# Kernel optimization log

Measured on AMD Instinct MI355X. Metric: run time of the kernel, lower is better.

## Reference

```python
import jax, jax.numpy as jnp
import numpy as np

EPS = 1e-8

@jax.custom_vjp
def spike(x):
    # Heaviside forward, SuperSpike surrogate gradient in backward
    return (x > 0.0).astype(x.dtype)

def _spike_fwd(x):
    return spike(x), x

def _spike_bwd(x, g):
    return (g / (1.0 + 10.0 * jnp.abs(x)) ** 2,)

spike.defvjp(_spike_fwd, _spike_bwd)


def setup_inputs() -> dict:
    key = jax.random.key(0)
    k1, k2, k3, k4 = jax.random.split(key, 4)
    B, T, I, O = 128, 128, 1024, 1024
    x = jax.random.normal(k1, (B, T, I), dtype=jnp.float32)
    # w ~ N(0, 1/sqrt(I)) per reset_parameters
    w = jax.random.normal(k2, (I, O), dtype=jnp.float32) * np.float32(1.0 / np.sqrt(I))
    # beta ~ N(0.7, 0.01), clamped to [0,1]
    beta = jnp.clip(0.7 + 0.01 * jax.random.normal(k3, (1,), dtype=jnp.float32), 0.0, 1.0)
    # b ~ N(1.0, 0.01), clamped to >= 0
    b = jnp.clip(1.0 + 0.01 * jax.random.normal(k4, (1024,), dtype=jnp.float32), 0.0, None)
    return {"x": x, "w": w, "beta": beta, "b": b}


def reference(x, w, beta, b):
    # x: [B, T, I]; w: [I, O]; beta: [1]; b: [O]
    h = jnp.einsum('btc,cd->btd', x, w)                 # [B, T, O]
    d = jnp.einsum('ab,ac->bc', w, w)                    # lateral reset matrix [O, O]
    norm = (w ** 2).sum(0)                               # [O]
    inv_norm = 1.0 / (norm + EPS)
    B, O = x.shape[0], w.shape[1]

    def step(carry, h_t):
        mem, spk = carry
        rst = spk @ d                                    # [B, O]
        mem = (mem - rst) * beta + h_t * (1.0 - beta)
        mthr = mem * inv_norm - b
        spk = spike(mthr)
        return (mem, spk), spk

    init = (jnp.zeros((B, O), x.dtype), jnp.zeros((B, O), x.dtype))
    _, spk_rec = jax.lax.scan(step, init, jnp.swapaxes(h, 0, 1))  # [T, B, O]
    spk_rec = jnp.swapaxes(spk_rec, 0, 1)                # [B, T, O]
    loss = 0.5 * (spk_rec ** 2).mean()
    return spk_rec, loss
```

## Files before the change

kernel.cpp:

```cpp
#include <hip/hip_runtime.h>
#include <hip/hip_fp16.h>

#define B_ 128
#define T_ 128
#define I_ 1024
#define O_ 1024
#define M_ (B_*T_)
#define NOUT (M_*O_)

typedef __attribute__((ext_vector_type(8))) _Float16 half8;
typedef __attribute__((ext_vector_type(4))) float floatx4;

__device__ __forceinline__ void gld_lds16(const void* g, void* l) {
    __builtin_amdgcn_global_load_lds((const __attribute__((address_space(1))) void*)g,
                                     (__attribute__((address_space(3))) void*)l,
                                     16, 0, 0);
}

__device__ __forceinline__ void barrier_lds_only() {
    asm volatile("" ::: "memory");
    __builtin_amdgcn_s_waitcnt(0xC07F);
    __builtin_amdgcn_s_barrier();
    asm volatile("" ::: "memory");
}

__device__ __forceinline__ void split3h(float x, unsigned short& h,
                                        unsigned short& m, unsigned short& l) {
    __half f0 = __float2half(x);
    float r1 = x - __half2float(f0);
    __half f1 = __float2half(r1);
    float r2 = r1 - __half2float(f1);
    __half f2 = __float2half(r2);
    h = __half_as_ushort(f0);
    m = __half_as_ushort(f1);
    l = __half_as_ushort(f2);
}

__global__ __launch_bounds__(256) void split_x(const float* __restrict__ X,
                                               unsigned short* __restrict__ Xh,
                                               unsigned short* __restrict__ Xm,
                                               unsigned short* __restrict__ Xl) {
    size_t base = ((size_t)blockIdx.x * 256 + threadIdx.x) * 4;
    float4 v = *(const float4*)(X + base);
    ushort4 hh, mm, ll;
    split3h(v.x, hh.x, mm.x, ll.x);
    split3h(v.y, hh.y, mm.y, ll.y);
    split3h(v.z, hh.z, mm.z, ll.z);
    split3h(v.w, hh.w, mm.w, ll.w);
    *(ushort4*)(Xh + base) = hh;
    *(ushort4*)(Xm + base) = mm;
    *(ushort4*)(Xl + base) = ll;
}

__global__ __launch_bounds__(256) void split_wt(const float* __restrict__ W,
                                                unsigned short* __restrict__ WTh,
                                                unsigned short* __restrict__ WTm,
                                                unsigned short* __restrict__ WTl) {
    __shared__ float t[64][65];
    const int tid = threadIdx.x;
    const int tx = tid & 63, ty4 = tid >> 6;
    const int r0 = blockIdx.x * 64, c0 = blockIdx.y * 64;
#pragma unroll
    for (int j = 0; j < 16; ++j) {
        int row = j * 4 + ty4;
        t[row][tx] = W[(size_t)(r0 + row) * O_ + c0 + tx];
    }
    __syncthreads();
#pragma unroll
    for (int j = 0; j < 16; ++j) {
        int i = j * 4 + ty4;
        float v = t[tx][i];
        unsigned short h, m, l;
        split3h(v, h, m, l);
        size_t off = (size_t)(c0 + i) * I_ + r0 + tx;
        WTh[off] = h; WTm[off] = m; WTl[off] = l;
    }
}

__global__ __launch_bounds__(512, 2) void gemm_h_mfma(
        const unsigned short* __restrict__ Xh, const unsigned short* __restrict__ Xm,
        const unsigned short* __restrict__ Xl, const unsigned short* __restrict__ WTh,
        const unsigned short* __restrict__ WTm, const unsigned short* __restrict__ WTl,
        float* __restrict__ H) {
    const int K = I_, N = O_;
    __shared__ unsigned short P[2][36864];

    const int tid = threadIdx.x;
    const int lane = tid & 63;
    const int wid = tid >> 6;
    const int wrow = wid >> 2;
    const int wcol = wid & 3;
    const int l15 = lane & 15, quad = lane >> 4;
    const int bm = blockIdx.x * 128, bn = blockIdx.y * 256;

    const int srow = tid >> 2, sch = tid & 3;
    const int schg = sch ^ ((srow >> 1) & 3);
    const unsigned short* gsrcA[3];
    const unsigned short* gsrcB[3];
    gsrcA[0] = Xh  + (size_t)(bm + srow) * K + schg * 8;
    gsrcA[1] = Xm  + (size_t)(bm + srow) * K + schg * 8;
    gsrcA[2] = Xl  + (size_t)(bm + srow) * K + schg * 8;
    gsrcB[0] = WTh + (size_t)(bn + srow) * K + schg * 8;
    gsrcB[1] = WTm + (size_t)(bn + srow) * K + schg * 8;
    gsrcB[2] = WTl + (size_t)(bn + srow) * K + schg * 8;

    auto stage = [&](int kt) {
        unsigned short* wb = &P[0][0] + (size_t)(kt & 1) * 36864;
        const size_t k0 = (size_t)kt * 32;
#pragma unroll
        for (int p = 0; p < 3; ++p)
            gld_lds16(gsrcA[p] + k0, wb + p * 4096 + tid * 8);
#pragma unroll
        for (int p = 0; p < 3; ++p) {
            unsigned short* bb = wb + 12288 + p * 8192 + tid * 8;
            gld_lds16(gsrcB[p] + k0, bb);
            gld_lds16(gsrcB[p] + (size_t)128 * K + k0, bb + 4096);
        }
    };

    floatx4 acc[4][4];
#pragma unroll
    for (int mt = 0; mt < 4; ++mt)
#pragma unroll
        for (int nt = 0; nt < 4; ++nt) acc[mt][nt] = (floatx4)(0.f);

    stage(0);

    for (int kt = 0; kt < 32; ++kt) {
        const unsigned short* rb = &P[0][0] + (size_t)(kt & 1) * 36864;

        asm volatile("" ::: "memory");
        __builtin_amdgcn_s_waitcnt(0x1F70);
        __builtin_amdgcn_s_barrier();
        asm volatile("" ::: "memory");

        half8 Af[3][4];
#pragma unroll
        for (int pa = 0; pa < 3; ++pa)
#pragma unroll
            for (int mt = 0; mt < 4; ++mt) {
                const int row = wrow * 64 + mt * 16 + l15;
                const int chk = quad ^ ((row >> 1) & 3);
                Af[pa][mt] = *(const half8*)(rb + pa * 4096 + row * 32 + chk * 8);
            }

        if (kt < 31) stage(kt + 1);

#pragma unroll
        for (int pb = 0; pb < 3; ++pb) {
            half8 Bf[4];
#pragma unroll
            for (int nt = 0; nt < 4; ++nt) {
                const int col = wcol * 64 + nt * 16 + l15;
                const int chk = quad ^ ((col >> 1) & 3);
                Bf[nt] = *(const half8*)(rb + 12288 + pb * 8192 + col * 32 + chk * 8);
            }
#pragma unroll
            for (int nt = 0; nt < 4; ++nt)
#pragma unroll
                for (int mt = 0; mt < 4; ++mt) {
                    acc[mt][nt] = __builtin_amdgcn_mfma_f32_16x16x32_f16(Af[0][mt], Bf[nt], acc[mt][nt], 0, 0, 0);
                    if (pb < 2)
                        acc[mt][nt] = __builtin_amdgcn_mfma_f32_16x16x32_f16(Af[1][mt], Bf[nt], acc[mt][nt], 0, 0, 0);
                    if (pb == 0)
                        acc[mt][nt] = __builtin_amdgcn_mfma_f32_16x16x32_f16(Af[2][mt], Bf[nt], acc[mt][nt], 0, 0, 0);
                }
        }
    }

#pragma unroll
    for (int mt = 0; mt < 4; ++mt)
#pragma unroll
        for (int nt = 0; nt < 4; ++nt) {
            int grow = bm + wrow * 64 + mt * 16 + quad * 4;
            int gcol = bn + wcol * 64 + nt * 16 + l15;
            float* hp = H + (size_t)grow * N + gcol;
#pragma unroll
            for (int r = 0; r < 4; ++r) hp[(size_t)r * N] = acc[mt][nt][r];
        }
}

__global__ __launch_bounds__(256) void gemm_wtw(const float* __restrict__ W,
                                                float* __restrict__ D) {
    const int K = I_, N = O_;
    __shared__ float As[32][68];
    __shared__ float Bs[32][68];
    const int tid = threadIdx.x;
    const int tx = tid & 15, ty = tid >> 4;
    const int bj = blockIdx.x * 64, bo = blockIdx.y * 64;
    const int lr = tid >> 4;
    const int lc = (tid & 15) << 2;

    float acc[4][4];
#pragma unroll
    for (int m = 0; m < 4; m++)
#pragma unroll
        for (int n = 0; n < 4; n++) acc[m][n] = 0.f;

    for (int k0 = 0; k0 < K; k0 += 32) {
        float4 a0 = *(const float4*)(W + (size_t)(k0 + lr) * N + bj + lc);
        float4 a1 = *(const float4*)(W + (size_t)(k0 + lr + 16) * N + bj + lc);
        float4 b0 = *(const float4*)(W + (size_t)(k0 + lr) * N + bo + lc);
        float4 b1 = *(const float4*)(W + (size_t)(k0 + lr + 16) * N + bo + lc);
        __syncthreads();
        *(float4*)&As[lr][lc] = a0; *(float4*)&As[lr + 16][lc] = a1;
        *(float4*)&Bs[lr][lc] = b0; *(float4*)&Bs[lr + 16][lc] = b1;
        __syncthreads();
#pragma unroll
        for (int k = 0; k < 32; ++k) {
            float4 av = *(const float4*)&As[k][ty * 4];
            float4 bv = *(const float4*)&Bs[k][tx * 4];
            float am[4] = {av.x, av.y, av.z, av.w};
            float bb[4] = {bv.x, bv.y, bv.z, bv.w};
#pragma unroll
            for (int m = 0; m < 4; m++)
#pragma unroll
                for (int n = 0; n < 4; n++) acc[m][n] += am[m] * bb[n];
        }
    }
#pragma unroll
    for (int m = 0; m < 4; m++) {
        float4 v = make_float4(acc[m][0], acc[m][1], acc[m][2], acc[m][3]);
        *(float4*)(D + (size_t)(bj + ty * 4 + m) * N + bo + tx * 4) = v;
    }
}

__global__ void colnorm_diag(const float* __restrict__ D, float* __restrict__ invn,
                             unsigned int* __restrict__ counter) {
    int o = blockIdx.x * 256 + threadIdx.x;
    if (o == 0) *counter = 0u;
    invn[o] = 1.0f / (D[(size_t)o * O_ + o] + 1e-8f);
}

__global__ __launch_bounds__(256) void scan_kernel(const float* __restrict__ h,
                                                   const float* __restrict__ d,
                                                   const float* __restrict__ invn,
                                                   const float* __restrict__ bias,
                                                   const float* __restrict__ beta,
                                                   float* __restrict__ out,
                                                   unsigned int* __restrict__ spike_count) {
    __shared__ int lst[2][O_];
    __shared__ int cnt[T_ + 1];
    __shared__ unsigned int red[256];

    const int tid = threadIdx.x;
    const int lane = tid & 63;
    const int b = blockIdx.x;
    const int o4 = tid * 4;
    const float betav = beta[0];
    const float omb = 1.0f - betav;

    const float4 invn4 = *(const float4*)(invn + o4);
    const float4 b4 = *(const float4*)(bias + o4);
    float4 mem4 = make_float4(0.f, 0.f, 0.f, 0.f);

    for (int i = tid; i <= T_; i += 256) cnt[i] = 0;
    unsigned int local_count = 0;
    const float* hb = h + (size_t)b * T_ * O_;
    float* ob = out + (size_t)b * T_ * O_;
    const unsigned long long below = (lane == 63) ? 0xFFFFFFFFFFFFFFFFull >> 1
                                                  : ((1ull << lane) - 1ull);

    float4 hcur = *(const float4*)(hb + o4);
    __syncthreads();

    for (int t = 0; t < T_; ++t) {
        const int p = t & 1, q = p ^ 1;
        const int n = cnt[t];

        float4 hnext = make_float4(0.f, 0.f, 0.f, 0.f);
        if (t + 1 < T_) hnext = *(const float4*)(hb + (size_t)(t + 1) * O_ + o4);

        float4 rst = make_float4(0.f, 0.f, 0.f, 0.f);
        int i = 0;
        for (; i + 16 <= n; i += 16) {
            float4 v[16];
#pragma unroll
            for (int u = 0; u < 16; ++u) {
                const int j = lst[p][i + u];
                v[u] = *(const float4*)(d + (size_t)j * O_ + o4);
            }
#pragma unroll
            for (int u = 0; u < 16; ++u) {
                rst.x += v[u].x; rst.y += v[u].y;
                rst.z += v[u].z; rst.w += v[u].w;
            }
        }
        for (; i + 4 <= n; i += 4) {
            float4 v[4];
#pragma unroll
            for (int u = 0; u < 4; ++u) {
                const int j = lst[p][i + u];
                v[u] = *(const float4*)(d + (size_t)j * O_ + o4);
            }
#pragma unroll
            for (int u = 0; u < 4; ++u) {
                rst.x += v[u].x; rst.y += v[u].y;
                rst.z += v[u].z; rst.w += v[u].w;
            }
        }
        for (; i < n; ++i) {
            const int j = lst[p][i];
            float4 v = *(const float4*)(d + (size_t)j * O_ + o4);
            rst.x += v.x; rst.y += v.y; rst.z += v.z; rst.w += v.w;
        }

        mem4.x = (mem4.x - rst.x) * betav + hcur.x * omb;
        mem4.y = (mem4.y - rst.y) * betav + hcur.y * omb;
        mem4.z = (mem4.z - rst.z) * betav + hcur.z * omb;
        mem4.w = (mem4.w - rst.w) * betav + hcur.w * omb;

        const int s[4] = {(mem4.x * invn4.x - b4.x) > 0.0f,
                          (mem4.y * invn4.y - b4.y) > 0.0f,
                          (mem4.z * invn4.z - b4.z) > 0.0f,
                          (mem4.w * invn4.w - b4.w) > 0.0f};

        float4 sv = make_float4(s[0] ? 1.f : 0.f, s[1] ? 1.f : 0.f,
                                s[2] ? 1.f : 0.f, s[3] ? 1.f : 0.f);
        *(float4*)(ob + (size_t)t * O_ + o4) = sv;
        local_count += (unsigned)(s[0] + s[1] + s[2] + s[3]);

        unsigned long long mk0 = __ballot(s[0]);
        unsigned long long mk1 = __ballot(s[1]);
        unsigned long long mk2 = __ballot(s[2]);
        unsigned long long mk3 = __ballot(s[3]);
        const int c0 = __popcll(mk0), c1 = __popcll(mk1), c2 = __popcll(mk2);
        const int tot = c0 + c1 + c2 + __popcll(mk3);
        int base = 0;
        if (lane == 0 && tot) base = atomicAdd(&cnt[t + 1], tot);
        base = __shfl(base, 0, 64);
        if (s[0]) lst[q][base + __popcll(mk0 & below)] = o4 + 0;
        base += c0;
        if (s[1]) lst[q][base + __popcll(mk1 & below)] = o4 + 1;
        base += c1;
        if (s[2]) lst[q][base + __popcll(mk2 & below)] = o4 + 2;
        base += c2;
        if (s[3]) lst[q][base + __popcll(mk3 & below)] = o4 + 3;

        barrier_lds_only();
        hcur = hnext;
    }

    red[tid] = local_count;
    __syncthreads();
    for (int st = 128; st > 0; st >>= 1) {
        if (tid < st) red[tid] += red[tid + st];
        __syncthreads();
    }
    if (tid == 0) atomicAdd(spike_count, red[0]);
}

__global__ void finalize_loss(const unsigned int* __restrict__ spike_count,
                              float* __restrict__ loss_out) {
    *loss_out = 0.5f * ((float)(*spike_count) / 16777216.0f);
}

extern "C" void kernel_launch(void* const* d_in, const int* in_sizes, int n_in,
                              void* d_out, int out_size, void* d_ws, size_t ws_size,
                              hipStream_t stream) {
    const float* x    = (const float*)d_in[0];
    const float* w    = (const float*)d_in[1];
    const float* beta = (const float*)d_in[2];
    const float* bias = (const float*)d_in[3];
    float* out = (float*)d_out;

    char* ws = (char*)d_ws;
    float* h    = (float*)ws;
    float* dmat = (float*)(ws + (size_t)67108864);
    float* invn = (float*)(ws + (size_t)71303168);
    unsigned int* cntp = (unsigned int*)(ws + (size_t)71307264);
    unsigned short* wt_h = (unsigned short*)(ws + (size_t)71311360);
    unsigned short* wt_m = (unsigned short*)(ws + (size_t)73408512);
    unsigned short* wt_l = (unsigned short*)(ws + (size_t)75505664);
    unsigned short* x_h  = (unsigned short*)(ws + (size_t)77602816);
    unsigned short* x_m  = (unsigned short*)(ws + (size_t)111157248);
    unsigned short* x_l  = (unsigned short*)(ws + (size_t)144711680);

    split_x<<<M_ * I_ / 1024, 256, 0, stream>>>(x, x_h, x_m, x_l);
    split_wt<<<dim3(I_ / 64, O_ / 64), 256, 0, stream>>>(w, wt_h, wt_m, wt_l);
    gemm_h_mfma<<<dim3(M_ / 128, O_ / 256), 512, 0, stream>>>(x_h, x_m, x_l,
                                                              wt_h, wt_m, wt_l, h);
    gemm_wtw<<<dim3(O_ / 64, O_ / 64), 256, 0, stream>>>(w, dmat);
    colnorm_diag<<<O_ / 256, 256, 0, stream>>>(dmat, invn, cntp);
    scan_kernel<<<B_, 256, 0, stream>>>(h, dmat, invn, bias, beta, out, cntp);
    finalize_loss<<<1, 1, 0, stream>>>(cntp, out + (size_t)NOUT);
}
```

Baseline: 456.3 us.

## Reuse MFMA split-precision GEMM for W^T W and widen scan to 512 threads

Drops the scalar FP32 tiled kernel for the lateral reset matrix and instead runs the existing split-fp16 MFMA GEMM on the transposed weight pieces, so D = W^T W uses matrix cores. The recurrent scan kernel now uses 512 threads per batch row, each owning two output neurons instead of four. That halves per-thread serial gather work on the spike lists and adds more waves to hide memory latency, at the cost of more barrier participants and smaller per-thread loads. The MFMA path relies on the three-way fp16 split to keep D accurate enough for the spike thresholds.

```diff
diff --git a/kernel.cpp b/kernel.cpp
--- a/kernel.cpp
+++ b/kernel.cpp
@@ -180,51 +180,6 @@
         }
 }
 
-__global__ __launch_bounds__(256) void gemm_wtw(const float* __restrict__ W,
-                                                float* __restrict__ D) {
-    const int K = I_, N = O_;
-    __shared__ float As[32][68];
-    __shared__ float Bs[32][68];
-    const int tid = threadIdx.x;
-    const int tx = tid & 15, ty = tid >> 4;
-    const int bj = blockIdx.x * 64, bo = blockIdx.y * 64;
-    const int lr = tid >> 4;
-    const int lc = (tid & 15) << 2;
-
-    float acc[4][4];
-#pragma unroll
-    for (int m = 0; m < 4; m++)
-#pragma unroll
-        for (int n = 0; n < 4; n++) acc[m][n] = 0.f;
-
-    for (int k0 = 0; k0 < K; k0 += 32) {
-        float4 a0 = *(const float4*)(W + (size_t)(k0 + lr) * N + bj + lc);
-        float4 a1 = *(const float4*)(W + (size_t)(k0 + lr + 16) * N + bj + lc);
-        float4 b0 = *(const float4*)(W + (size_t)(k0 + lr) * N + bo + lc);
-        float4 b1 = *(const float4*)(W + (size_t)(k0 + lr + 16) * N + bo + lc);
-        __syncthreads();
-        *(float4*)&As[lr][lc] = a0; *(float4*)&As[lr + 16][lc] = a1;
-        *(float4*)&Bs[lr][lc] = b0; *(float4*)&Bs[lr + 16][lc] = b1;
-        __syncthreads();
-#pragma unroll
-        for (int k = 0; k < 32; ++k) {
-            float4 av = *(const float4*)&As[k][ty * 4];
-            float4 bv = *(const float4*)&Bs[k][tx * 4];
-            float am[4] = {av.x, av.y, av.z, av.w};
-            float bb[4] = {bv.x, bv.y, bv.z, bv.w};
-#pragma unroll
-            for (int m = 0; m < 4; m++)
-#pragma unroll
-                for (int n = 0; n < 4; n++) acc[m][n] += am[m] * bb[n];
-        }
-    }
-#pragma unroll
-    for (int m = 0; m < 4; m++) {
-        float4 v = make_float4(acc[m][0], acc[m][1], acc[m][2], acc[m][3]);
-        *(float4*)(D + (size_t)(bj + ty * 4 + m) * N + bo + tx * 4) = v;
-    }
-}
-
 __global__ void colnorm_diag(const float* __restrict__ D, float* __restrict__ invn,
                              unsigned int* __restrict__ counter) {
     int o = blockIdx.x * 256 + threadIdx.x;
@@ -232,7 +187,7 @@
     invn[o] = 1.0f / (D[(size_t)o * O_ + o] + 1e-8f);
 }
 
-__global__ __launch_bounds__(256) void scan_kernel(const float* __restrict__ h,
+__global__ __launch_bounds__(512) void scan_kernel(const float* __restrict__ h,
                                                    const float* __restrict__ d,
                                                    const float* __restrict__ invn,
                                                    const float* __restrict__ bias,
@@ -241,101 +196,84 @@
                                                    unsigned int* __restrict__ spike_count) {
     __shared__ int lst[2][O_];
     __shared__ int cnt[T_ + 1];
-    __shared__ unsigned int red[256];
+    __shared__ unsigned int red[512];
 
     const int tid = threadIdx.x;
     const int lane = tid & 63;
     const int b = blockIdx.x;
-    const int o4 = tid * 4;
+    const int o2 = tid * 2;
     const float betav = beta[0];
     const float omb = 1.0f - betav;
 
-    const float4 invn4 = *(const float4*)(invn + o4);
-    const float4 b4 = *(const float4*)(bias + o4);
-    float4 mem4 = make_float4(0.f, 0.f, 0.f, 0.f);
-
-    for (int i = tid; i <= T_; i += 256) cnt[i] = 0;
+    const float2 invn2 = *(const float2*)(invn + o2);
+    const float2 b2 = *(const float2*)(bias + o2);
+    float2 mem2 = make_float2(0.f, 0.f);
+
+    for (int i = tid; i <= T_; i += 512) cnt[i] = 0;
     unsigned int local_count = 0;
     const float* hb = h + (size_t)b * T_ * O_;
     float* ob = out + (size_t)b * T_ * O_;
     const unsigned long long below = (lane == 63) ? 0xFFFFFFFFFFFFFFFFull >> 1
                                                   : ((1ull << lane) - 1ull);
 
-    float4 hcur = *(const float4*)(hb + o4);
+    float2 hcur = *(const float2*)(hb + o2);
     __syncthreads();
 
     for (int t = 0; t < T_; ++t) {
         const int p = t & 1, q = p ^ 1;
         const int n = cnt[t];
 
-        float4 hnext = make_float4(0.f, 0.f, 0.f, 0.f);
-        if (t + 1 < T_) hnext = *(const float4*)(hb + (size_t)(t + 1) * O_ + o4);
-
-        float4 rst = make_float4(0.f, 0.f, 0.f, 0.f);
+        float2 hnext = make_float2(0.f, 0.f);
+        if (t + 1 < T_) hnext = *(const float2*)(hb + (size_t)(t + 1) * O_ + o2);
+
+        float2 rst = make_float2(0.f, 0.f);
         int i = 0;
         for (; i + 16 <= n; i += 16) {
-            float4 v[16];
+            float2 v[16];
 #pragma unroll
             for (int u = 0; u < 16; ++u) {
                 const int j = lst[p][i + u];
-                v[u] = *(const float4*)(d + (size_t)j * O_ + o4);
+                v[u] = *(const float2*)(d + (size_t)j * O_ + o2);
             }
 #pragma unroll
-            for (int u = 0; u < 16; ++u) {
-                rst.x += v[u].x; rst.y += v[u].y;
-                rst.z += v[u].z; rst.w += v[u].w;
-            }
+            for (int u = 0; u < 16; ++u) { rst.x += v[u].x; rst.y += v[u].y; }
         }
         for (; i + 4 <= n; i += 4) {
-            float4 v[4];
+            float2 v[4];
 #pragma unroll
             for (int u = 0; u < 4; ++u) {
                 const int j = lst[p][i + u];
-                v[u] = *(const float4*)(d + (size_t)j * O_ + o4);
+                v[u] = *(const float2*)(d + (size_t)j * O_ + o2);
             }
 #pragma unroll
-            for (int u = 0; u < 4; ++u) {
-                rst.x += v[u].x; rst.y += v[u].y;
-                rst.z += v[u].z; rst.w += v[u].w;
-            }
+            for (int u = 0; u < 4; ++u) { rst.x += v[u].x; rst.y += v[u].y; }
         }
         for (; i < n; ++i) {
             const int j = lst[p][i];
-            float4 v = *(const float4*)(d + (size_t)j * O_ + o4);
-            rst.x += v.x; rst.y += v.y; rst.z += v.z; rst.w += v.w;
-        }
-
-        mem4.x = (mem4.x - rst.x) * betav + hcur.x * omb;
-        mem4.y = (mem4.y - rst.y) * betav + hcur.y * omb;
-        mem4.z = (mem4.z - rst.z) * betav + hcur.z * omb;
-        mem4.w = (mem4.w - rst.w) * betav + hcur.w * omb;
-
-        const int s[4] = {(mem4.x * invn4.x - b4.x) > 0.0f,
-                          (mem4.y * invn4.y - b4.y) > 0.0f,
-                          (mem4.z * invn4.z - b4.z) > 0.0f,
-                          (mem4.w * invn4.w - b4.w) > 0.0f};
-
-        float4 sv = make_float4(s[0] ? 1.f : 0.f, s[1] ? 1.f : 0.f,
-                                s[2] ? 1.f : 0.f, s[3] ? 1.f : 0.f);
-        *(float4*)(ob + (size_t)t * O_ + o4) = sv;
-        local_count += (unsigned)(s[0] + s[1] + s[2] + s[3]);
-
-        unsigned long long mk0 = __ballot(s[0]);
-        unsigned long long mk1 = __ballot(s[1]);
-        unsigned long long mk2 = __ballot(s[2]);
-        unsigned long long mk3 = __ballot(s[3]);
-        const int c0 = __popcll(mk0), c1 = __popcll(mk1), c2 = __popcll(mk2);
-        const int tot = c0 + c1 + c2 + __popcll(mk3);
+            float2 v = *(const float2*)(d + (size_t)j * O_ + o2);
+            rst.x += v.x; rst.y += v.y;
+        }
+
+        mem2.x = (mem2.x - rst.x) * betav + hcur.x * omb;
+        mem2.y = (mem2.y - rst.y) * betav + hcur.y * omb;
+
+        const int s0 = (mem2.x * invn2.x - b2.x) > 0.0f;
+        const int s1 = (mem2.y * invn2.y - b2.y) > 0.0f;
+
+        float2 sv = make_float2(s0 ? 1.f : 0.f, s1 ? 1.f : 0.f);
+        *(float2*)(ob + (size_t)t * O_ + o2) = sv;
+        local_count += (unsigned)(s0 + s1);
+
+        unsigned long long mk0 = __ballot(s0);
+        unsigned long long mk1 = __ballot(s1);
+        const int c0 = __popcll(mk0);
+        const int tot = c0 + __popcll(mk1);
         int base = 0;
         if (lane == 0 && tot) base = atomicAdd(&cnt[t + 1], tot);
         base = __shfl(base, 0, 64);
-        if (s[0]) lst[q][base + __popcll(mk0 & below)] = o4 + 0;
+        if (s0) lst[q][base + __popcll(mk0 & below)] = o2 + 0;
         base += c0;
-        if (s[1]) lst[q][base + __popcll(mk1 & below)] = o4 + 1;
-        base += c1;
-        if (s[2]) lst[q][base + __popcll(mk2 & below)] = o4 + 2;
-        base += c2;
-        if (s[3]) lst[q][base + __popcll(mk3 & below)] = o4 + 3;
+        if (s1) lst[q][base + __popcll(mk1 & below)] = o2 + 1;
 
         barrier_lds_only();
         hcur = hnext;
@@ -343,7 +281,7 @@
 
     red[tid] = local_count;
     __syncthreads();
-    for (int st = 128; st > 0; st >>= 1) {
+    for (int st = 256; st > 0; st >>= 1) {
         if (tid < st) red[tid] += red[tid + st];
         __syncthreads();
     }
@@ -380,8 +318,9 @@
     split_wt<<<dim3(I_ / 64, O_ / 64), 256, 0, stream>>>(w, wt_h, wt_m, wt_l);
     gemm_h_mfma<<<dim3(M_ / 128, O_ / 256), 512, 0, stream>>>(x_h, x_m, x_l,
                                                               wt_h, wt_m, wt_l, h);
-    gemm_wtw<<<dim3(O_ / 64, O_ / 64), 256, 0, stream>>>(w, dmat);
+    gemm_h_mfma<<<dim3(O_ / 128, O_ / 256), 512, 0, stream>>>(wt_h, wt_m, wt_l,
+                                                              wt_h, wt_m, wt_l, dmat);
     colnorm_diag<<<O_ / 256, 256, 0, stream>>>(dmat, invn, cntp);
-    scan_kernel<<<B_, 256, 0, stream>>>(h, dmat, invn, bias, beta, out, cntp);
+    scan_kernel<<<B_, 512, 0, stream>>>(h, dmat, invn, bias, beta, out, cntp);
     finalize_loss<<<1, 1, 0, stream>>>(cntp, out + (size_t)NOUT);
 }
```

After: 478.8 us. +4.9%, slower.
